# Kernel optimization log

Hardware: AMD Instinct MI355X
Metric: run time of the kernel (lower is better)

Reference implementation:

```python
import jax, jax.numpy as jnp
import numpy as np

B, Hs, Ws, DIM = 8, 32, 32, 768
NH, HD = 12, 64  # num_heads, head_dim


def get_rel_pos(size, rel_pos):
    # q_size == k_size == size; no interpolation branch needed
    coords = jnp.arange(size)[:, None] - jnp.arange(size)[None, :] + (size - 1)
    return rel_pos[coords]  # (size, size, head_dim)


def setup_inputs() -> dict:
    key = jax.random.key(0)
    ks = jax.random.split(key, 7)
    inv = 1.0 / np.sqrt(DIM)
    return {
        "x": jax.random.normal(ks[0], (B, Hs, Ws, DIM), jnp.float32),
        "qkv_w": jax.random.normal(ks[1], (3 * DIM, DIM), jnp.float32) * inv,
        "qkv_b": jax.random.normal(ks[2], (3 * DIM,), jnp.float32) * 0.02,
        "proj_w": jax.random.normal(ks[3], (DIM, DIM), jnp.float32) * inv,
        "proj_b": jax.random.normal(ks[4], (DIM,), jnp.float32) * 0.02,
        "rel_pos_h": jax.random.normal(ks[5], (2 * Hs - 1, HD), jnp.float32) * 0.02,
        "rel_pos_w": jax.random.normal(ks[6], (2 * Ws - 1, HD), jnp.float32) * 0.02,
    }


def reference(x, qkv_w, qkv_b, proj_w, proj_b, rel_pos_h, rel_pos_w):
    Bb, H, W, C = x.shape
    L = H * W
    scale = HD ** -0.5

    qkv = x @ qkv_w.T + qkv_b                       # (B,H,W,3C)
    qkv = qkv.reshape(Bb, L, 3, NH, HD).transpose(2, 0, 3, 1, 4)
    q, k, v = qkv[0], qkv[1], qkv[2]                # (B,NH,L,HD)

    # decomposed 2D relative position bias
    rel_h = get_rel_pos(H, rel_pos_h)               # (H,H,HD)
    rel_w = get_rel_pos(W, rel_pos_w)               # (W,W,HD)
    q5 = q.reshape(Bb, NH, H, W, HD)
    rel_h_attn = jnp.einsum('bnhwc,hkc->bnhwk', q5, rel_h)  # (B,NH,H,W,H)
    rel_w_attn = jnp.einsum('bnhwc,wkc->bnhwk', q5, rel_w)  # (B,NH,H,W,W)
    bias = rel_h_attn[..., :, None] + rel_w_attn[..., None, :]  # (B,NH,H,W,H,W)
    bias = bias.reshape(Bb, NH, L, L)

    scores = jnp.einsum('bnqd,bnkd->bnqk', q, k) * scale + bias
    attn = jax.nn.softmax(scores, axis=-1)
    out = jnp.einsum('bnqk,bnkd->bnqd', attn, v)    # (B,NH,L,HD)

    out = out.reshape(Bb, NH, H, W, HD).transpose(0, 2, 3, 1, 4).reshape(Bb, H, W, C)
    return out @ proj_w.T + proj_b
```

## Files before the change

### kernel.cpp

```cpp
#include <hip/hip_runtime.h>

typedef unsigned short u16;
typedef __bf16 bf16x8 __attribute__((ext_vector_type(8)));
typedef float f32x4 __attribute__((ext_vector_type(4)));

#define NHEAD 12
#define LQ 1024
#define HDIM 64
#define DIMM 768

__device__ __forceinline__ u16 f2b(float f) {
  unsigned u = __float_as_uint(f);
  u += 0x7fffu + ((u >> 16) & 1u);
  return (u16)(u >> 16);
}
__device__ __forceinline__ float b2f(u16 v) {
  return __uint_as_float(((unsigned)v) << 16);
}
__device__ __forceinline__ unsigned cvt_pk(float lo, float hi) {
  unsigned r;
  asm("v_cvt_pk_bf16_f32 %0, %1, %2" : "=v"(r) : "v"(lo), "v"(hi));
  return r;
}
__device__ __forceinline__ void async16(const void* g, void* l) {
  __builtin_amdgcn_global_load_lds(
      (const __attribute__((address_space(1))) void*)g,
      (__attribute__((address_space(3))) void*)l, 16, 0, 0);
}
__device__ __forceinline__ uint2 shfl_u2(uint2 v, int src) {
  uint2 r;
  r.x = (unsigned)__shfl((int)v.x, src, 64);
  r.y = (unsigned)__shfl((int)v.y, src, 64);
  return r;
}

__global__ __launch_bounds__(256) void cvt_kernel(const float* __restrict__ in,
                                                  u16* __restrict__ out, int n4) {
  int i = blockIdx.x * 256 + threadIdx.x;
  if (i >= n4) return;
  const float4 v = reinterpret_cast<const float4*>(in)[i];
  ushort4 o;
  o.x = f2b(v.x); o.y = f2b(v.y); o.z = f2b(v.z); o.w = f2b(v.w);
  reinterpret_cast<ushort4*>(out)[i] = o;
}

__global__ __launch_bounds__(256) void cvt_rel(const float* __restrict__ rph,
                                               const float* __restrict__ rpw,
                                               u16* __restrict__ rphb,
                                               u16* __restrict__ rpwb) {
  int i = blockIdx.x * 256 + threadIdx.x;
  int tab = i >> 12, idx = i & 4095;
  int m = idx >> 6, d = idx & 63;
  const float* src = tab ? rpw : rph;
  u16* dst = tab ? rpwb : rphb;
  dst[idx] = (m < 63) ? f2b(src[m * HDIM + d]) : (u16)0;
}

__global__ __launch_bounds__(256) void gemm_qkv(const u16* __restrict__ A,
                                                const u16* __restrict__ Bt,
                                                const float* __restrict__ bias,
                                                u16* __restrict__ qb,
                                                u16* __restrict__ kb,
                                                u16* __restrict__ vtb) {
  __shared__ u16 la[2][128 * 64];
  __shared__ u16 lb[2][128 * 64];
  const int K = DIMM;
  int t = threadIdx.x;
  int lane = t & 63, wv = t >> 6;
  int l15 = lane & 15, l4 = lane >> 4;
  int swz = (blockIdx.x & 7) * 144 + (blockIdx.x >> 3);
  int bm = swz / 18, bn = swz % 18;
  int m0 = bm * 128, n0 = bn * 128;
  int wm = (wv >> 1) * 64, wn = (wv & 1) * 64;

  auto stage = [&](int s, int buf) {
    int k0 = s * 64;
    #pragma unroll
    for (int i = 0; i < 4; ++i) {
      int c = i * 256 + t;
      int row = c >> 3, co = c & 7;
      int g = co ^ (row & 7);
      async16(A + (m0 + row) * K + k0 + g * 8, (char*)&la[buf][0] + c * 16);
      async16(Bt + (n0 + row) * K + k0 + g * 8, (char*)&lb[buf][0] + c * 16);
    }
  };

  f32x4 acc[4][4];
  #pragma unroll
  for (int i = 0; i < 4; ++i)
    #pragma unroll
    for (int j = 0; j < 4; ++j) acc[i][j] = {0.f, 0.f, 0.f, 0.f};

  stage(0, 0);
  #pragma unroll 2
  for (int s = 0; s < 12; ++s) {
    int cur = s & 1;
    __syncthreads();
    if (s + 1 < 12) stage(s + 1, cur ^ 1);
    bf16x8 af[4][2], bfr[4][2];
    #pragma unroll
    for (int mi = 0; mi < 4; ++mi) {
      int row = wm + mi * 16 + l15;
      #pragma unroll
      for (int ks2 = 0; ks2 < 2; ++ks2)
        af[mi][ks2] = *reinterpret_cast<const bf16x8*>(
            &la[cur][row * 64 + (((ks2 << 2) + l4) ^ (row & 7)) * 8]);
    }
    #pragma unroll
    for (int nj = 0; nj < 4; ++nj) {
      int row = wn + nj * 16 + l15;
      #pragma unroll
      for (int ks2 = 0; ks2 < 2; ++ks2)
        bfr[nj][ks2] = *reinterpret_cast<const bf16x8*>(
            &lb[cur][row * 64 + (((ks2 << 2) + l4) ^ (row & 7)) * 8]);
    }
    #pragma unroll
    for (int mi = 0; mi < 4; ++mi)
      #pragma unroll
      for (int nj = 0; nj < 4; ++nj)
        #pragma unroll
        for (int ks2 = 0; ks2 < 2; ++ks2)
          acc[mi][nj] = __builtin_amdgcn_mfma_f32_16x16x32_bf16(
              af[mi][ks2], bfr[nj][ks2], acc[mi][nj], 0, 0, 0);
  }

  int part = (n0 >> 7) / 6;
  if (part < 2) {
    #pragma unroll
    for (int nj = 0; nj < 4; ++nj) {
      int n = n0 + wn + nj * 16 + l15;
      float bv = bias[n];
      int d = n & 63;
      int head = (n >> 6) % NHEAD;
      #pragma unroll
      for (int mi = 0; mi < 4; ++mi) {
        #pragma unroll
        for (int r = 0; r < 4; ++r) {
          int m = m0 + wm + mi * 16 + l4 * 4 + r;
          int b = m >> 10, li = m & 1023;
          int bh = b * NHEAD + head;
          u16 o = f2b(acc[mi][nj][r] + bv);
          if (part == 0) qb[(bh * LQ + li) * HDIM + d] = o;
          else           kb[(bh * LQ + li) * HDIM + d] = o;
        }
      }
    }
  } else {
    __syncthreads();
    u16* tile = &la[0][0];
    #pragma unroll
    for (int nj = 0; nj < 4; ++nj) {
      int rowl = wn + nj * 16 + l15;
      float bv = bias[n0 + rowl];
      #pragma unroll
      for (int mi = 0; mi < 4; ++mi) {
        int col4 = (wm + mi * 16 + l4 * 4) >> 2;
        int col4s = col4 ^ ((rowl & 7) << 2);
        ushort4 o;
        o.x = f2b(acc[mi][nj][0] + bv);
        o.y = f2b(acc[mi][nj][1] + bv);
        o.z = f2b(acc[mi][nj][2] + bv);
        o.w = f2b(acc[mi][nj][3] + bv);
        *reinterpret_cast<ushort4*>(&tile[rowl * 128 + col4s * 4]) = o;
      }
    }
    __syncthreads();
    int b = m0 >> 10;
    int vn0 = n0 - 1536;
    #pragma unroll
    for (int i = 0; i < 8; ++i) {
      int c = i * 256 + t;
      int rowl = c >> 4, col16 = c & 15;
      int col4s = (col16 * 2) ^ ((rowl & 7) << 2);
      uint4 v = *reinterpret_cast<const uint4*>(&tile[rowl * 128 + col4s * 4]);
      int vn = vn0 + rowl;
      int bh = b * NHEAD + (vn >> 6);
      int d = vn & 63;
      int li0 = (m0 & 1023) + col16 * 8;
      *reinterpret_cast<uint4*>(&vtb[(bh * HDIM + d) * LQ + li0]) = v;
    }
  }
}

__global__ __launch_bounds__(256) void attn_kernel(const u16* __restrict__ qb,
                                                   const u16* __restrict__ kb,
                                                   const u16* __restrict__ vtb,
                                                   const u16* __restrict__ rphb,
                                                   const u16* __restrict__ rpwb,
                                                   u16* __restrict__ ao) {
  __shared__ u16 lds_k[2][64 * 64];
  __shared__ u16 lds_v[2][64 * 64];
  __shared__ u16 lds_th[64 * 72];
  __shared__ u16 lds_tw[64 * 72];

  int swz = (blockIdx.x & 7) * 192 + (blockIdx.x >> 3);
  int bh = swz >> 4;
  int q0 = (swz & 15) * 64;
  int t = threadIdx.x;
  int wv = t >> 6, lane = t & 63;
  int l15 = lane & 15, l4 = lane >> 4;

  auto stagekv = [&](int kv0, int buf) {
    const u16* ks = kb + (bh * LQ + kv0) * HDIM;
    const u16* vs = vtb + bh * HDIM * LQ + kv0;
    #pragma unroll
    for (int i = 0; i < 2; ++i) {
      int c = i * 256 + t;
      int row = c >> 3, co = c & 7;
      int g = co ^ (row & 7);
      async16(ks + row * HDIM + g * 8, (char*)&lds_k[buf][0] + c * 16);
      async16(vs + row * LQ + g * 8, (char*)&lds_v[buf][0] + c * 16);
    }
  };

  stagekv(0, 0);

  bf16x8 qf[2];
  {
    const u16* qsrc = qb + (bh * LQ + q0 + wv * 16 + l15) * HDIM + l4 * 8;
    qf[0] = *reinterpret_cast<const bf16x8*>(qsrc);
    qf[1] = *reinterpret_cast<const bf16x8*>(qsrc + 32);
  }

  #pragma unroll
  for (int c = 0; c < 4; ++c) {
    f32x4 th = {0.f, 0.f, 0.f, 0.f}, tw = {0.f, 0.f, 0.f, 0.f};
    #pragma unroll
    for (int ks2 = 0; ks2 < 2; ++ks2) {
      bf16x8 bhf = *reinterpret_cast<const bf16x8*>(&rphb[(c * 16 + l15) * HDIM + ks2 * 32 + l4 * 8]);
      bf16x8 bwf = *reinterpret_cast<const bf16x8*>(&rpwb[(c * 16 + l15) * HDIM + ks2 * 32 + l4 * 8]);
      th = __builtin_amdgcn_mfma_f32_16x16x32_bf16(qf[ks2], bhf, th, 0, 0, 0);
      tw = __builtin_amdgcn_mfma_f32_16x16x32_bf16(qf[ks2], bwf, tw, 0, 0, 0);
    }
    #pragma unroll
    for (int r = 0; r < 4; ++r) {
      int row = wv * 16 + l4 * 4 + r;
      lds_th[row * 72 + c * 16 + l15] = f2b(th[r]);
      lds_tw[row * 72 + c * 16 + l15] = f2b(tw[r]);
    }
  }

  int gq = q0 + wv * 16 + l15;
  int hq = gq >> 5, wq = gq & 31;
  int lrow = wv * 16 + l15;
  const u16* thp = &lds_th[lrow * 72 + hq + 31];
  const u16* twp = &lds_tw[lrow * 72 + wq + 31];

  float tw_reg[8];
  #pragma unroll
  for (int j = 0; j < 8; ++j) {
    int k2 = (j >> 2) * 16 + l4 * 4 + (j & 3);
    tw_reg[j] = b2f(twp[-k2]);
  }

  float m_run = -1e30f, l_run = 0.f;
  f32x4 acc_o[4];
  #pragma unroll
  for (int dj = 0; dj < 4; ++dj) acc_o[dj] = {0.f, 0.f, 0.f, 0.f};

  int srcA = l15 + (l4 & 1) * 32;
  int srcB = srcA + 16;
  bool hiG = (l4 >> 1) & 1;

  #pragma unroll 2
  for (int cidx = 0; cidx < 16; ++cidx) {
    int cur = cidx & 1;
    int kv0 = cidx * 64;
    __syncthreads();
    if (cidx + 1 < 16) stagekv(kv0 + 64, cur ^ 1);

    f32x4 sc[4];
    __builtin_amdgcn_s_setprio(1);
    #pragma unroll
    for (int nj = 0; nj < 4; ++nj) {
      f32x4 a = {0.f, 0.f, 0.f, 0.f};
      #pragma unroll
      for (int ks2 = 0; ks2 < 2; ++ks2) {
        int co = (ks2 * 4 + l4) ^ (l15 & 7);
        bf16x8 kf = *reinterpret_cast<const bf16x8*>(&lds_k[cur][(nj * 16 + l15) * 64 + co * 8]);
        a = __builtin_amdgcn_mfma_f32_16x16x32_bf16(kf, qf[ks2], a, 0, 0, 0);
      }
      sc[nj] = a;
    }
    __builtin_amdgcn_s_setprio(0);

    int kv5 = kv0 >> 5;
    float th0 = b2f(thp[-kv5]);
    float th1 = b2f(thp[-kv5 - 1]);
    float p[4][4];
    float cmax = -1e30f;
    #pragma unroll
    for (int nj = 0; nj < 4; ++nj) {
      float thv = (nj < 2) ? th0 : th1;
      #pragma unroll
      for (int r = 0; r < 4; ++r) {
        float s = fmaf(sc[nj][r], 0.125f, thv) + tw_reg[(nj & 1) * 4 + r];
        p[nj][r] = s;
        cmax = fmaxf(cmax, s);
      }
    }
    cmax = fmaxf(cmax, __shfl_xor(cmax, 16));
    cmax = fmaxf(cmax, __shfl_xor(cmax, 32));

    if (!__all(cmax <= m_run + 8.0f)) {
      float mn = fmaxf(m_run, cmax);
      float scl = __expf(m_run - mn);
      m_run = mn;
      l_run *= scl;
      #pragma unroll
      for (int dj = 0; dj < 4; ++dj)
        #pragma unroll
        for (int r = 0; r < 4; ++r) acc_o[dj][r] *= scl;
    }

    float psum = 0.f;
    #pragma unroll
    for (int nj = 0; nj < 4; ++nj)
      #pragma unroll
      for (int r = 0; r < 4; ++r) {
        p[nj][r] = __expf(p[nj][r] - m_run);
        psum += p[nj][r];
      }
    psum += __shfl_xor(psum, 16);
    psum += __shfl_xor(psum, 32);
    l_run += psum;

    uint2 w4[4];
    #pragma unroll
    for (int nj = 0; nj < 4; ++nj) {
      w4[nj].x = cvt_pk(p[nj][0], p[nj][1]);
      w4[nj].y = cvt_pk(p[nj][2], p[nj][3]);
    }
    bf16x8 pf[2];
    #pragma unroll
    for (int ks2 = 0; ks2 < 2; ++ks2) {
      uint2 lo0 = shfl_u2(w4[ks2 * 2 + 0], srcA);
      uint2 lo1 = shfl_u2(w4[ks2 * 2 + 1], srcA);
      uint2 hi0 = shfl_u2(w4[ks2 * 2 + 0], srcB);
      uint2 hi1 = shfl_u2(w4[ks2 * 2 + 1], srcB);
      union { uint4 u; bf16x8 b; } cv;
      cv.u.x = hiG ? lo1.x : lo0.x;
      cv.u.y = hiG ? lo1.y : lo0.y;
      cv.u.z = hiG ? hi1.x : hi0.x;
      cv.u.w = hiG ? hi1.y : hi0.y;
      pf[ks2] = cv.b;
    }

    __builtin_amdgcn_s_setprio(1);
    #pragma unroll
    for (int dj = 0; dj < 4; ++dj) {
      int d = dj * 16 + l15;
      #pragma unroll
      for (int ks2 = 0; ks2 < 2; ++ks2) {
        int co = (ks2 * 4 + l4) ^ (l15 & 7);
        bf16x8 vf = *reinterpret_cast<const bf16x8*>(&lds_v[cur][d * 64 + co * 8]);
        acc_o[dj] = __builtin_amdgcn_mfma_f32_16x16x32_bf16(vf, pf[ks2], acc_o[dj], 0, 0, 0);
      }
    }
    __builtin_amdgcn_s_setprio(0);
  }

  int b = bh / NHEAD, head = bh % NHEAD;
  float inv = 1.f / l_run;
  u16* orow = ao + (b * LQ + gq) * DIMM + head * HDIM;
  #pragma unroll
  for (int dj = 0; dj < 4; ++dj) {
    uint2 pk;
    pk.x = cvt_pk(acc_o[dj][0] * inv, acc_o[dj][1] * inv);
    pk.y = cvt_pk(acc_o[dj][2] * inv, acc_o[dj][3] * inv);
    *reinterpret_cast<uint2*>(&orow[dj * 16 + l4 * 4]) = pk;
  }
}

__global__ __launch_bounds__(256) void gemm_proj(const u16* __restrict__ A,
                                                 const u16* __restrict__ Bt,
                                                 const float* __restrict__ bias,
                                                 float* __restrict__ out) {
  __shared__ u16 la[2][128 * 64];
  __shared__ u16 lb[2][128 * 64];
  const int K = DIMM;
  int t = threadIdx.x;
  int lane = t & 63, wv = t >> 6;
  int l15 = lane & 15, l4 = lane >> 4;
  int swz = (blockIdx.x & 7) * 48 + (blockIdx.x >> 3);
  int bm = swz / 6, bn = swz % 6;
  int m0 = bm * 128, n0 = bn * 128;
  int wm = (wv >> 1) * 64, wn = (wv & 1) * 64;

  auto stage = [&](int s, int buf) {
    int k0 = s * 64;
    #pragma unroll
    for (int i = 0; i < 4; ++i) {
      int c = i * 256 + t;
      int row = c >> 3, co = c & 7;
      int g = co ^ (row & 7);
      async16(A + (m0 + row) * K + k0 + g * 8, (char*)&la[buf][0] + c * 16);
      async16(Bt + (n0 + row) * K + k0 + g * 8, (char*)&lb[buf][0] + c * 16);
    }
  };

  f32x4 acc[4][4];
  #pragma unroll
  for (int i = 0; i < 4; ++i)
    #pragma unroll
    for (int j = 0; j < 4; ++j) acc[i][j] = {0.f, 0.f, 0.f, 0.f};

  stage(0, 0);
  #pragma unroll 2
  for (int s = 0; s < 12; ++s) {
    int cur = s & 1;
    __syncthreads();
    if (s + 1 < 12) stage(s + 1, cur ^ 1);
    bf16x8 af[4][2], bfr[4][2];
    #pragma unroll
    for (int mi = 0; mi < 4; ++mi) {
      int row = wm + mi * 16 + l15;
      #pragma unroll
      for (int ks2 = 0; ks2 < 2; ++ks2)
        af[mi][ks2] = *reinterpret_cast<const bf16x8*>(
            &la[cur][row * 64 + (((ks2 << 2) + l4) ^ (row & 7)) * 8]);
    }
    #pragma unroll
    for (int nj = 0; nj < 4; ++nj) {
      int row = wn + nj * 16 + l15;
      #pragma unroll
      for (int ks2 = 0; ks2 < 2; ++ks2)
        bfr[nj][ks2] = *reinterpret_cast<const bf16x8*>(
            &lb[cur][row * 64 + (((ks2 << 2) + l4) ^ (row & 7)) * 8]);
    }
    #pragma unroll
    for (int mi = 0; mi < 4; ++mi)
      #pragma unroll
      for (int nj = 0; nj < 4; ++nj)
        #pragma unroll
        for (int ks2 = 0; ks2 < 2; ++ks2)
          acc[mi][nj] = __builtin_amdgcn_mfma_f32_16x16x32_bf16(
              af[mi][ks2], bfr[nj][ks2], acc[mi][nj], 0, 0, 0);
  }

  #pragma unroll
  for (int nj = 0; nj < 4; ++nj) {
    int n = n0 + wn + nj * 16 + l15;
    float bv = bias[n];
    #pragma unroll
    for (int mi = 0; mi < 4; ++mi) {
      #pragma unroll
      for (int r = 0; r < 4; ++r) {
        int m = m0 + wm + mi * 16 + l4 * 4 + r;
        out[m * DIMM + n] = acc[mi][nj][r] + bv;
      }
    }
  }
}

extern "C" void kernel_launch(void* const* d_in, const int* in_sizes, int n_in,
                              void* d_out, int out_size, void* d_ws, size_t ws_size,
                              hipStream_t stream) {
  const float* x      = (const float*)d_in[0];
  const float* qkv_w  = (const float*)d_in[1];
  const float* qkv_b  = (const float*)d_in[2];
  const float* proj_w = (const float*)d_in[3];
  const float* proj_b = (const float*)d_in[4];
  const float* rph    = (const float*)d_in[5];
  const float* rpw    = (const float*)d_in[6];
  float* out = (float*)d_out;
  char* ws = (char*)d_ws;

  u16*   xb     = (u16*)(ws + 0);
  u16*   wqkvb  = (u16*)(ws + 12582912);
  u16*   wprojb = (u16*)(ws + 16121856);
  u16*   qb     = (u16*)(ws + 17301504);
  u16*   kb     = (u16*)(ws + 29884416);
  u16*   vtb    = (u16*)(ws + 42467328);
  u16*   rphb   = (u16*)(ws + 55050240);
  u16*   rpwb   = (u16*)(ws + 55058432);
  u16*   ao     = xb;

  cvt_kernel<<<6144, 256, 0, stream>>>(x, xb, 8192 * 768 / 4);
  cvt_kernel<<<1728, 256, 0, stream>>>(qkv_w, wqkvb, 2304 * 768 / 4);
  cvt_kernel<<<576, 256, 0, stream>>>(proj_w, wprojb, 768 * 768 / 4);
  cvt_rel<<<32, 256, 0, stream>>>(rph, rpw, rphb, rpwb);

  gemm_qkv<<<64 * 18, 256, 0, stream>>>(xb, wqkvb, qkv_b, qb, kb, vtb);

  attn_kernel<<<96 * 16, 256, 0, stream>>>(qb, kb, vtb, rphb, rpwb, ao);

  gemm_proj<<<64 * 6, 256, 0, stream>>>(ao, wprojb, proj_b, out);
}
```

Measured before the change: 149.4 us.

## Process two query row groups per attention block and switch softmax to exp2

Each attention block now handles 128 query rows (two 64-row groups per wave set) instead of 64, so every K/V tile staged into LDS feeds twice as many MFMAs and grid size halves. The relative-position tables are pre-scaled by log2(e) so the softmax uses exp2 directly, and the bias tables are stored compactly, keeping only the 32 entries each row needs. This cuts K/V global traffic and per-tile sync overhead per query, but doubles accumulator and score registers, which may lower occupancy, and leaves fewer blocks to spread across CUs.

```diff
diff --git a/kernel.cpp b/kernel.cpp
--- a/kernel.cpp
+++ b/kernel.cpp
@@ -8,6 +8,7 @@
 #define LQ 1024
 #define HDIM 64
 #define DIMM 768
+#define LOG2E 1.44269504088896f
 
 __device__ __forceinline__ u16 f2b(float f) {
   unsigned u = __float_as_uint(f);
@@ -53,7 +54,7 @@
   int m = idx >> 6, d = idx & 63;
   const float* src = tab ? rpw : rph;
   u16* dst = tab ? rpwb : rphb;
-  dst[idx] = (m < 63) ? f2b(src[m * HDIM + d]) : (u16)0;
+  dst[idx] = (m < 63) ? f2b(src[m * HDIM + d] * LOG2E) : (u16)0;
 }
 
 __global__ __launch_bounds__(256) void gemm_qkv(const u16* __restrict__ A,
@@ -190,12 +191,12 @@
                                                    u16* __restrict__ ao) {
   __shared__ u16 lds_k[2][64 * 64];
   __shared__ u16 lds_v[2][64 * 64];
-  __shared__ u16 lds_th[64 * 72];
-  __shared__ u16 lds_tw[64 * 72];
-
-  int swz = (blockIdx.x & 7) * 192 + (blockIdx.x >> 3);
-  int bh = swz >> 4;
-  int q0 = (swz & 15) * 64;
+  __shared__ u16 th_c[128 * 36];
+  __shared__ u16 tw_c[128 * 36];
+
+  int swz = (blockIdx.x & 7) * 96 + (blockIdx.x >> 3);
+  int bh = swz >> 3;
+  int q0 = (swz & 7) * 128;
   int t = threadIdx.x;
   int wv = t >> 6, lane = t & 63;
   int l15 = lane & 15, l4 = lane >> 4;
@@ -215,136 +216,159 @@
 
   stagekv(0, 0);
 
-  bf16x8 qf[2];
-  {
-    const u16* qsrc = qb + (bh * LQ + q0 + wv * 16 + l15) * HDIM + l4 * 8;
-    qf[0] = *reinterpret_cast<const bf16x8*>(qsrc);
-    qf[1] = *reinterpret_cast<const bf16x8*>(qsrc + 32);
-  }
-
-  #pragma unroll
-  for (int c = 0; c < 4; ++c) {
-    f32x4 th = {0.f, 0.f, 0.f, 0.f}, tw = {0.f, 0.f, 0.f, 0.f};
-    #pragma unroll
-    for (int ks2 = 0; ks2 < 2; ++ks2) {
-      bf16x8 bhf = *reinterpret_cast<const bf16x8*>(&rphb[(c * 16 + l15) * HDIM + ks2 * 32 + l4 * 8]);
-      bf16x8 bwf = *reinterpret_cast<const bf16x8*>(&rpwb[(c * 16 + l15) * HDIM + ks2 * 32 + l4 * 8]);
-      th = __builtin_amdgcn_mfma_f32_16x16x32_bf16(qf[ks2], bhf, th, 0, 0, 0);
-      tw = __builtin_amdgcn_mfma_f32_16x16x32_bf16(qf[ks2], bwf, tw, 0, 0, 0);
-    }
-    #pragma unroll
-    for (int r = 0; r < 4; ++r) {
-      int row = wv * 16 + l4 * 4 + r;
-      lds_th[row * 72 + c * 16 + l15] = f2b(th[r]);
-      lds_tw[row * 72 + c * 16 + l15] = f2b(tw[r]);
-    }
-  }
-
-  int gq = q0 + wv * 16 + l15;
-  int hq = gq >> 5, wq = gq & 31;
-  int lrow = wv * 16 + l15;
-  const u16* thp = &lds_th[lrow * 72 + hq + 31];
-  const u16* twp = &lds_tw[lrow * 72 + wq + 31];
-
-  float tw_reg[8];
-  #pragma unroll
-  for (int j = 0; j < 8; ++j) {
-    int k2 = (j >> 2) * 16 + l4 * 4 + (j & 3);
-    tw_reg[j] = b2f(twp[-k2]);
-  }
-
-  float m_run = -1e30f, l_run = 0.f;
-  f32x4 acc_o[4];
-  #pragma unroll
-  for (int dj = 0; dj < 4; ++dj) acc_o[dj] = {0.f, 0.f, 0.f, 0.f};
+  bf16x8 qf[2][2];
+  #pragma unroll
+  for (int rg = 0; rg < 2; ++rg) {
+    const u16* qsrc = qb + (bh * LQ + q0 + rg * 64 + wv * 16 + l15) * HDIM + l4 * 8;
+    qf[rg][0] = *reinterpret_cast<const bf16x8*>(qsrc);
+    qf[rg][1] = *reinterpret_cast<const bf16x8*>(qsrc + 32);
+  }
+
+  #pragma unroll
+  for (int rg = 0; rg < 2; ++rg) {
+    int rowbase = rg * 64 + wv * 16;
+    int hqb = (q0 + rowbase) >> 5;
+    #pragma unroll
+    for (int c = 0; c < 4; ++c) {
+      f32x4 th = {0.f, 0.f, 0.f, 0.f}, tw = {0.f, 0.f, 0.f, 0.f};
+      #pragma unroll
+      for (int ks2 = 0; ks2 < 2; ++ks2) {
+        bf16x8 bhf = *reinterpret_cast<const bf16x8*>(&rphb[(c * 16 + l15) * HDIM + ks2 * 32 + l4 * 8]);
+        bf16x8 bwf = *reinterpret_cast<const bf16x8*>(&rpwb[(c * 16 + l15) * HDIM + ks2 * 32 + l4 * 8]);
+        th = __builtin_amdgcn_mfma_f32_16x16x32_bf16(qf[rg][ks2], bhf, th, 0, 0, 0);
+        tw = __builtin_amdgcn_mfma_f32_16x16x32_bf16(qf[rg][ks2], bwf, tw, 0, 0, 0);
+      }
+      int mcol = c * 16 + l15;
+      #pragma unroll
+      for (int r = 0; r < 4; ++r) {
+        int lrow = rowbase + l4 * 4 + r;
+        int jh = mcol - hqb;
+        if ((unsigned)jh < 32u) th_c[lrow * 36 + jh] = f2b(th[r]);
+        int jw = mcol - (lrow & 31);
+        if ((unsigned)jw < 32u) tw_c[lrow * 36 + jw] = f2b(tw[r]);
+      }
+    }
+  }
+
+  int row36[2];
+  float tw_reg[2][8];
+  #pragma unroll
+  for (int rg = 0; rg < 2; ++rg) {
+    row36[rg] = (rg * 64 + wv * 16 + l15) * 36;
+    #pragma unroll
+    for (int j = 0; j < 8; ++j) {
+      int k2 = (j >> 2) * 16 + l4 * 4 + (j & 3);
+      tw_reg[rg][j] = b2f(tw_c[row36[rg] + 31 - k2]);
+    }
+  }
+
+  float m_run[2] = {-1e30f, -1e30f}, l_run[2] = {0.f, 0.f};
+  f32x4 acc0[4], acc1[4];
+  #pragma unroll
+  for (int dj = 0; dj < 4; ++dj) { acc0[dj] = {0.f, 0.f, 0.f, 0.f}; acc1[dj] = {0.f, 0.f, 0.f, 0.f}; }
 
   int srcA = l15 + (l4 & 1) * 32;
   int srcB = srcA + 16;
   bool hiG = (l4 >> 1) & 1;
+  const float SCL = 0.125f * LOG2E;
 
   #pragma unroll 2
   for (int cidx = 0; cidx < 16; ++cidx) {
     int cur = cidx & 1;
-    int kv0 = cidx * 64;
     __syncthreads();
-    if (cidx + 1 < 16) stagekv(kv0 + 64, cur ^ 1);
-
-    f32x4 sc[4];
+    if (cidx + 1 < 16) stagekv(cidx * 64 + 64, cur ^ 1);
+
+    f32x4 sc[2][4];
     __builtin_amdgcn_s_setprio(1);
     #pragma unroll
     for (int nj = 0; nj < 4; ++nj) {
-      f32x4 a = {0.f, 0.f, 0.f, 0.f};
+      f32x4 a0 = {0.f, 0.f, 0.f, 0.f}, a1 = {0.f, 0.f, 0.f, 0.f};
       #pragma unroll
       for (int ks2 = 0; ks2 < 2; ++ks2) {
         int co = (ks2 * 4 + l4) ^ (l15 & 7);
         bf16x8 kf = *reinterpret_cast<const bf16x8*>(&lds_k[cur][(nj * 16 + l15) * 64 + co * 8]);
-        a = __builtin_amdgcn_mfma_f32_16x16x32_bf16(kf, qf[ks2], a, 0, 0, 0);
-      }
-      sc[nj] = a;
+        a0 = __builtin_amdgcn_mfma_f32_16x16x32_bf16(kf, qf[0][ks2], a0, 0, 0, 0);
+        a1 = __builtin_amdgcn_mfma_f32_16x16x32_bf16(kf, qf[1][ks2], a1, 0, 0, 0);
+      }
+      sc[0][nj] = a0; sc[1][nj] = a1;
     }
     __builtin_amdgcn_s_setprio(0);
 
-    int kv5 = kv0 >> 5;
-    float th0 = b2f(thp[-kv5]);
-    float th1 = b2f(thp[-kv5 - 1]);
-    float p[4][4];
-    float cmax = -1e30f;
-    #pragma unroll
-    for (int nj = 0; nj < 4; ++nj) {
-      float thv = (nj < 2) ? th0 : th1;
-      #pragma unroll
-      for (int r = 0; r < 4; ++r) {
-        float s = fmaf(sc[nj][r], 0.125f, thv) + tw_reg[(nj & 1) * 4 + r];
-        p[nj][r] = s;
-        cmax = fmaxf(cmax, s);
-      }
-    }
-    cmax = fmaxf(cmax, __shfl_xor(cmax, 16));
-    cmax = fmaxf(cmax, __shfl_xor(cmax, 32));
-
-    if (!__all(cmax <= m_run + 8.0f)) {
-      float mn = fmaxf(m_run, cmax);
-      float scl = __expf(m_run - mn);
-      m_run = mn;
-      l_run *= scl;
-      #pragma unroll
-      for (int dj = 0; dj < 4; ++dj)
+    int jbase = 30 - cidx * 2;
+    uint2 w4[2][4];
+    #pragma unroll
+    for (int rg = 0; rg < 2; ++rg) {
+      unsigned thw = *reinterpret_cast<const unsigned*>(&th_c[row36[rg] + jbase]);
+      float th1 = b2f((u16)thw);
+      float th0 = b2f((u16)(thw >> 16));
+      float p[4][4];
+      float cmax = -1e30f;
+      #pragma unroll
+      for (int nj = 0; nj < 4; ++nj) {
+        float thv = (nj < 2) ? th0 : th1;
         #pragma unroll
-        for (int r = 0; r < 4; ++r) acc_o[dj][r] *= scl;
-    }
-
-    float psum = 0.f;
-    #pragma unroll
-    for (int nj = 0; nj < 4; ++nj)
-      #pragma unroll
-      for (int r = 0; r < 4; ++r) {
-        p[nj][r] = __expf(p[nj][r] - m_run);
-        psum += p[nj][r];
-      }
-    psum += __shfl_xor(psum, 16);
-    psum += __shfl_xor(psum, 32);
-    l_run += psum;
-
-    uint2 w4[4];
-    #pragma unroll
-    for (int nj = 0; nj < 4; ++nj) {
-      w4[nj].x = cvt_pk(p[nj][0], p[nj][1]);
-      w4[nj].y = cvt_pk(p[nj][2], p[nj][3]);
-    }
-    bf16x8 pf[2];
-    #pragma unroll
-    for (int ks2 = 0; ks2 < 2; ++ks2) {
-      uint2 lo0 = shfl_u2(w4[ks2 * 2 + 0], srcA);
-      uint2 lo1 = shfl_u2(w4[ks2 * 2 + 1], srcA);
-      uint2 hi0 = shfl_u2(w4[ks2 * 2 + 0], srcB);
-      uint2 hi1 = shfl_u2(w4[ks2 * 2 + 1], srcB);
-      union { uint4 u; bf16x8 b; } cv;
-      cv.u.x = hiG ? lo1.x : lo0.x;
-      cv.u.y = hiG ? lo1.y : lo0.y;
-      cv.u.z = hiG ? hi1.x : hi0.x;
-      cv.u.w = hiG ? hi1.y : hi0.y;
-      pf[ks2] = cv.b;
-    }
+        for (int r = 0; r < 4; ++r) {
+          float s = fmaf(sc[rg][nj][r], SCL, thv) + tw_reg[rg][(nj & 1) * 4 + r];
+          p[nj][r] = s;
+          cmax = fmaxf(cmax, s);
+        }
+      }
+      cmax = fmaxf(cmax, __shfl_xor(cmax, 16));
+      cmax = fmaxf(cmax, __shfl_xor(cmax, 32));
+
+      if (!__all(cmax <= m_run[rg] + 11.5416f)) {
+        float mn = fmaxf(m_run[rg], cmax);
+        float scl = exp2f(m_run[rg] - mn);
+        m_run[rg] = mn;
+        l_run[rg] *= scl;
+        if (rg == 0) {
+          #pragma unroll
+          for (int dj = 0; dj < 4; ++dj)
+            #pragma unroll
+            for (int r = 0; r < 4; ++r) acc0[dj][r] *= scl;
+        } else {
+          #pragma unroll
+          for (int dj = 0; dj < 4; ++dj)
+            #pragma unroll
+            for (int r = 0; r < 4; ++r) acc1[dj][r] *= scl;
+        }
+      }
+
+      float psum = 0.f;
+      #pragma unroll
+      for (int nj = 0; nj < 4; ++nj)
+        #pragma unroll
+        for (int r = 0; r < 4; ++r) {
+          p[nj][r] = exp2f(p[nj][r] - m_run[rg]);
+          psum += p[nj][r];
+        }
+      psum += __shfl_xor(psum, 16);
+      psum += __shfl_xor(psum, 32);
+      l_run[rg] += psum;
+
+      #pragma unroll
+      for (int nj = 0; nj < 4; ++nj) {
+        w4[rg][nj].x = cvt_pk(p[nj][0], p[nj][1]);
+        w4[rg][nj].y = cvt_pk(p[nj][2], p[nj][3]);
+      }
+    }
+
+    bf16x8 pf[2][2];
+    #pragma unroll
+    for (int rg = 0; rg < 2; ++rg)
+      #pragma unroll
+      for (int ks2 = 0; ks2 < 2; ++ks2) {
+        uint2 lo0 = shfl_u2(w4[rg][ks2 * 2 + 0], srcA);
+        uint2 lo1 = shfl_u2(w4[rg][ks2 * 2 + 1], srcA);
+        uint2 hi0 = shfl_u2(w4[rg][ks2 * 2 + 0], srcB);
+        uint2 hi1 = shfl_u2(w4[rg][ks2 * 2 + 1], srcB);
+        union { uint4 u; bf16x8 b; } cv;
+        cv.u.x = hiG ? lo1.x : lo0.x;
+        cv.u.y = hiG ? lo1.y : lo0.y;
+        cv.u.z = hiG ? hi1.x : hi0.x;
+        cv.u.w = hiG ? hi1.y : hi0.y;
+        pf[rg][ks2] = cv.b;
+      }
 
     __builtin_amdgcn_s_setprio(1);
     #pragma unroll
@@ -354,21 +378,27 @@
       for (int ks2 = 0; ks2 < 2; ++ks2) {
         int co = (ks2 * 4 + l4) ^ (l15 & 7);
         bf16x8 vf = *reinterpret_cast<const bf16x8*>(&lds_v[cur][d * 64 + co * 8]);
-        acc_o[dj] = __builtin_amdgcn_mfma_f32_16x16x32_bf16(vf, pf[ks2], acc_o[dj], 0, 0, 0);
+        acc0[dj] = __builtin_amdgcn_mfma_f32_16x16x32_bf16(vf, pf[0][ks2], acc0[dj], 0, 0, 0);
+        acc1[dj] = __builtin_amdgcn_mfma_f32_16x16x32_bf16(vf, pf[1][ks2], acc1[dj], 0, 0, 0);
       }
     }
     __builtin_amdgcn_s_setprio(0);
   }
 
   int b = bh / NHEAD, head = bh % NHEAD;
-  float inv = 1.f / l_run;
-  u16* orow = ao + (b * LQ + gq) * DIMM + head * HDIM;
-  #pragma unroll
-  for (int dj = 0; dj < 4; ++dj) {
-    uint2 pk;
-    pk.x = cvt_pk(acc_o[dj][0] * inv, acc_o[dj][1] * inv);
-    pk.y = cvt_pk(acc_o[dj][2] * inv, acc_o[dj][3] * inv);
-    *reinterpret_cast<uint2*>(&orow[dj * 16 + l4 * 4]) = pk;
+  #pragma unroll
+  for (int rg = 0; rg < 2; ++rg) {
+    int gq = q0 + rg * 64 + wv * 16 + l15;
+    float inv = 1.f / l_run[rg];
+    u16* orow = ao + (b * LQ + gq) * DIMM + head * HDIM;
+    #pragma unroll
+    for (int dj = 0; dj < 4; ++dj) {
+      f32x4 a = rg ? acc1[dj] : acc0[dj];
+      uint2 pk;
+      pk.x = cvt_pk(a[0] * inv, a[1] * inv);
+      pk.y = cvt_pk(a[2] * inv, a[3] * inv);
+      *reinterpret_cast<uint2*>(&orow[dj * 16 + l4 * 4]) = pk;
+    }
   }
 }
 
@@ -483,7 +513,7 @@
 
   gemm_qkv<<<64 * 18, 256, 0, stream>>>(xb, wqkvb, qkv_b, qb, kb, vtb);
 
-  attn_kernel<<<96 * 16, 256, 0, stream>>>(qb, kb, vtb, rphb, rpwb, ao);
+  attn_kernel<<<96 * 8, 256, 0, stream>>>(qb, kb, vtb, rphb, rpwb, ao);
 
   gemm_proj<<<64 * 6, 256, 0, stream>>>(ao, wprojb, proj_b, out);
 }
```

New measurement: 160.2 us. 7.3% more time.
